# Kernel tuning notes

Hardware: AMD Instinct MI355X
Metric: run time of the kernel (lower is better)

The kernel has to match this reference:

```python
import jax, jax.numpy as jnp
import numpy as np

B, C, H, W = 8, 128, 64, 64
CQK = C // 8


def setup_inputs() -> dict:
    key = jax.random.key(0)
    ks = jax.random.split(key, 7)
    scale = 1.0 / np.sqrt(C)
    return {
        "x": jax.random.normal(ks[0], (B, C, H, W), dtype=jnp.float32),
        "wq": jax.random.normal(ks[1], (CQK, C), dtype=jnp.float32) * scale,
        "bq": jax.random.normal(ks[2], (CQK,), dtype=jnp.float32) * 0.01,
        "wk": jax.random.normal(ks[3], (CQK, C), dtype=jnp.float32) * scale,
        "bk": jax.random.normal(ks[4], (CQK,), dtype=jnp.float32) * 0.01,
        "wv": jax.random.normal(ks[5], (C, C), dtype=jnp.float32) * scale,
        "bv": jax.random.normal(ks[6], (C,), dtype=jnp.float32) * 0.01,
    }


def reference(x, wq, bq, wk, bk, wv, bv):
    b, c, h, w = x.shape
    n = h * w
    xf = x.reshape(b, c, n)                                  # [B,C,N]
    # 1x1 convs == channel matmuls
    q = jnp.einsum('oc,bcn->bon', wq, xf) + bq[:, None]      # [B,C/8,N]
    k = jnp.einsum('oc,bcn->bon', wk, xf) + bk[:, None]      # [B,C/8,N]
    v = jnp.einsum('oc,bcn->bon', wv, xf) + bv[:, None]      # [B,C,N]
    # energy[b,i,j] = <q[:,i], k[:,j]>  (note: NO 1/sqrt(d) scale, per source)
    energy = jnp.einsum('bci,bcj->bij', q, k)                # [B,N,N]
    att = jax.nn.softmax(energy, axis=-1)                    # softmax over j
    # out[b,c,i] = sum_j v[b,c,j] * att[b,i,j]
    out = jnp.einsum('bcj,bij->bci', v, att).reshape(b, c, h, w)
    return out + x
```

## Files before the change

### kernel.cpp

```cpp
#include <hip/hip_runtime.h>
#include <math.h>

#define NB  8
#define NC  128
#define NN  4096
#define NCQ 16
#define BI  64
#define BJ  64
#define WROWS 160

typedef __attribute__((ext_vector_type(8))) short short8v;
typedef __attribute__((ext_vector_type(4))) short short4v;
typedef __attribute__((ext_vector_type(4))) float f32x4;

__device__ __forceinline__ short f2bf(float f) {
    unsigned u = __builtin_bit_cast(unsigned, f);
    u += 0x7fffu + ((u >> 16) & 1u);
    return (short)(u >> 16);
}
__device__ __forceinline__ float bf2f(short h) {
    return __builtin_bit_cast(float, ((unsigned)(unsigned short)h) << 16);
}

__global__ __launch_bounds__(256) void qkv_proj(
    const float* __restrict__ x,
    const float* __restrict__ wq, const float* __restrict__ bq,
    const float* __restrict__ wk, const float* __restrict__ bk,
    const float* __restrict__ wv, const float* __restrict__ bv,
    short* __restrict__ Qo, short* __restrict__ Ko, short* __restrict__ Vo)
{
    __shared__ __align__(16) short wh[WROWS][NC];
    __shared__ __align__(16) short wl[WROWS][NC];
    __shared__ float bias_s[WROWS];

    const int b  = blockIdx.y;
    const int n0 = blockIdx.x * 128;
    const int t  = threadIdx.x;
    const int w  = t >> 6;
    const int l  = t & 63;
    const int lr = l & 15;
    const int g  = l >> 4;

    for (int idx = t; idx < (WROWS * NC) / 4; idx += 256) {
        const int row = idx >> 5;
        const int c4  = (idx & 31) * 4;
        const float* src = (row < 16) ? (wq + row * NC + c4)
                         : (row < 32) ? (wk + (row - 16) * NC + c4)
                                      : (wv + (row - 32) * NC + c4);
        const float4 v = *reinterpret_cast<const float4*>(src);
        short4v h4, l4;
        const float vf[4] = {v.x, v.y, v.z, v.w};
#pragma unroll
        for (int p = 0; p < 4; ++p) {
            const short hi = f2bf(vf[p]);
            h4[p] = hi;
            l4[p] = f2bf(vf[p] - bf2f(hi));
        }
        const int cs = c4 ^ ((row & 7) << 3);
        *reinterpret_cast<short4v*>(&wh[row][cs]) = h4;
        *reinterpret_cast<short4v*>(&wl[row][cs]) = l4;
    }
    for (int i = t; i < WROWS; i += 256)
        bias_s[i] = (i < 16) ? bq[i] : (i < 32) ? bk[i - 16] : bv[i - 32];
    __syncthreads();

    const int col0 = n0 + (2 * w) * 16 + lr;
    const int col1 = col0 + 16;
    const float* xb = x + (size_t)b * NC * NN;

    f32x4 acc[10][2];
#pragma unroll
    for (int rt = 0; rt < 10; ++rt)
#pragma unroll
        for (int c = 0; c < 2; ++c) acc[rt][c] = {0.f, 0.f, 0.f, 0.f};

#pragma unroll
    for (int ks = 0; ks < 4; ++ks) {
        short8v xh0, xl0, xh1, xl1;
        {
            const float* xp0 = xb + (size_t)(32 * ks + 8 * g) * NN + col0;
            const float* xp1 = xb + (size_t)(32 * ks + 8 * g) * NN + col1;
#pragma unroll
            for (int e = 0; e < 8; ++e) {
                const float f0 = xp0[(size_t)e * NN];
                const float f1 = xp1[(size_t)e * NN];
                const short h0 = f2bf(f0), h1 = f2bf(f1);
                xh0[e] = h0; xl0[e] = f2bf(f0 - bf2f(h0));
                xh1[e] = h1; xl1[e] = f2bf(f1 - bf2f(h1));
            }
        }
#pragma unroll
        for (int rt = 0; rt < 10; ++rt) {
            const int row = 16 * rt + lr;
            const int cs  = (32 * ks + 8 * g) ^ ((row & 7) << 3);
            const short8v ah = *reinterpret_cast<const short8v*>(&wh[row][cs]);
            const short8v al = *reinterpret_cast<const short8v*>(&wl[row][cs]);
            acc[rt][0] = __builtin_amdgcn_mfma_f32_16x16x32_bf16(ah, xh0, acc[rt][0], 0, 0, 0);
            acc[rt][0] = __builtin_amdgcn_mfma_f32_16x16x32_bf16(ah, xl0, acc[rt][0], 0, 0, 0);
            acc[rt][0] = __builtin_amdgcn_mfma_f32_16x16x32_bf16(al, xh0, acc[rt][0], 0, 0, 0);
            acc[rt][1] = __builtin_amdgcn_mfma_f32_16x16x32_bf16(ah, xh1, acc[rt][1], 0, 0, 0);
            acc[rt][1] = __builtin_amdgcn_mfma_f32_16x16x32_bf16(ah, xl1, acc[rt][1], 0, 0, 0);
            acc[rt][1] = __builtin_amdgcn_mfma_f32_16x16x32_bf16(al, xh1, acc[rt][1], 0, 0, 0);
        }
    }

#pragma unroll
    for (int rt = 0; rt < 10; ++rt) {
#pragma unroll
        for (int ctx = 0; ctx < 2; ++ctx) {
            const int col = (ctx == 0) ? col0 : col1;
#pragma unroll
            for (int r = 0; r < 4; ++r) {
                const int ch = 16 * rt + 4 * g + r;
                const short o = f2bf(acc[rt][ctx][r] + bias_s[ch]);
                if (rt == 0)
                    Qo[((size_t)b * NCQ + ch) * NN + col] = o;
                else if (rt == 1)
                    Ko[((size_t)b * NCQ + (ch - 16)) * NN + col] = o;
                else
                    Vo[((size_t)b * NC + (ch - 32)) * NN + col] = o;
            }
        }
    }
}

__global__ __launch_bounds__(256) void attn_mfma(
    const short* __restrict__ Q, const short* __restrict__ K,
    const short* __restrict__ V, const float* __restrict__ x,
    float* __restrict__ out)
{
    __shared__ __align__(16) short ksT[2][BJ * 24];
    __shared__ __align__(16) short vsT[2][NC * BJ];
    __shared__ __align__(16) short psT[4][16 * BJ];

    const int b  = blockIdx.y;
    const int i0 = blockIdx.x * BI;
    const int t  = threadIdx.x;
    const int w  = t >> 6;
    const int l  = t & 63;
    const int lr = l & 15;
    const int g  = l >> 4;
    const int swz = (lr & 7) << 3;

    const short* Qb = Q + (size_t)b * NCQ * NN;
    const short* Kb = K + (size_t)b * NCQ * NN;
    const short* Vb = V + (size_t)b * NC * NN;

    const int ig = i0 + 16 * w + lr;

    const short8v kzero = {0, 0, 0, 0, 0, 0, 0, 0};
    const f32x4   fzero = {0.f, 0.f, 0.f, 0.f};

    const int kc  = t >> 4;
    const int kj4 = (t & 15) * 4;
    const int vc0 = t >> 3;
    const int vj8 = (t & 7) * 8;

    short4v kreg;
    short8v vreg0, vreg1, vreg2, vreg3;

#define LOAD_TILE(J0)                                                            \
    {                                                                            \
        kreg  = *reinterpret_cast<const short4v*>(Kb + (size_t)kc * NN + (J0) + kj4); \
        vreg0 = *reinterpret_cast<const short8v*>(Vb + (size_t)(vc0      ) * NN + (J0) + vj8); \
        vreg1 = *reinterpret_cast<const short8v*>(Vb + (size_t)(vc0 + 32 ) * NN + (J0) + vj8); \
        vreg2 = *reinterpret_cast<const short8v*>(Vb + (size_t)(vc0 + 64 ) * NN + (J0) + vj8); \
        vreg3 = *reinterpret_cast<const short8v*>(Vb + (size_t)(vc0 + 96 ) * NN + (J0) + vj8); \
    }
#define WRITE_TILE(BUF)                                                          \
    {                                                                            \
        _Pragma("unroll")                                                        \
        for (int p = 0; p < 4; ++p) ksT[BUF][(kj4 + p) * 24 + kc] = kreg[p];     \
        const int sw0 = vj8 ^ ((vc0 & 7) << 3);                                  \
        *reinterpret_cast<short8v*>(&vsT[BUF][(vc0      ) * BJ + sw0]) = vreg0;  \
        *reinterpret_cast<short8v*>(&vsT[BUF][(vc0 + 32 ) * BJ + sw0]) = vreg1;  \
        *reinterpret_cast<short8v*>(&vsT[BUF][(vc0 + 64 ) * BJ + sw0]) = vreg2;  \
        *reinterpret_cast<short8v*>(&vsT[BUF][(vc0 + 96 ) * BJ + sw0]) = vreg3;  \
    }

    short8v qf = kzero;
    if (g < 2) {
        const short* qp = Qb + (size_t)(8 * g) * NN + ig;
#pragma unroll
        for (int e = 0; e < 8; ++e) qf[e] = qp[(size_t)e * NN];
    }

    float l_run = 0.f;
    f32x4 acc[8];
#pragma unroll
    for (int cb = 0; cb < 8; ++cb) acc[cb] = fzero;

    LOAD_TILE(0)
    WRITE_TILE(0)
    __syncthreads();

    for (int jt = 0; jt < NN / BJ; ++jt) {
        const int cur = jt & 1;
        if (jt < NN / BJ - 1) LOAD_TILE((jt + 1) * BJ)

        f32x4 e0, e1, e2, e3;
#define QK_TILE(ET, TT)                                                          \
        {                                                                        \
            short8v kf = kzero;                                                  \
            if (g < 2)                                                           \
                kf = *reinterpret_cast<const short8v*>(                          \
                        &ksT[cur][(16 * (TT) + lr) * 24 + 8 * g]);               \
            ET = __builtin_amdgcn_mfma_f32_16x16x32_bf16(kf, qf, fzero, 0, 0, 0);\
        }
        QK_TILE(e0, 0) QK_TILE(e1, 1) QK_TILE(e2, 2) QK_TILE(e3, 3)
#undef QK_TILE

        float sum = 0.f;
#pragma unroll
        for (int r = 0; r < 4; ++r) { e0[r] = __expf(e0[r]); sum += e0[r]; }
#pragma unroll
        for (int r = 0; r < 4; ++r) { e1[r] = __expf(e1[r]); sum += e1[r]; }
#pragma unroll
        for (int r = 0; r < 4; ++r) { e2[r] = __expf(e2[r]); sum += e2[r]; }
#pragma unroll
        for (int r = 0; r < 4; ++r) { e3[r] = __expf(e3[r]); sum += e3[r]; }
        sum += __shfl_xor(sum, 16);
        sum += __shfl_xor(sum, 32);
        l_run += sum;

#define P_STORE(ET, TT)                                                           \
        {                                                                         \
            const int jb = 16 * (TT) + 4 * g;                                     \
            unsigned p01 = (unsigned short)f2bf(ET[0]) |                          \
                           ((unsigned)(unsigned short)f2bf(ET[1]) << 16);         \
            unsigned p23 = (unsigned short)f2bf(ET[2]) |                          \
                           ((unsigned)(unsigned short)f2bf(ET[3]) << 16);         \
            *reinterpret_cast<unsigned*>(&psT[w][lr * BJ + ( jb      ^ swz)]) = p01; \
            *reinterpret_cast<unsigned*>(&psT[w][lr * BJ + ((jb + 2) ^ swz)]) = p23; \
        }
        P_STORE(e0, 0) P_STORE(e1, 1) P_STORE(e2, 2) P_STORE(e3, 3)
#undef P_STORE

        __builtin_amdgcn_s_setprio(1);
#pragma unroll
        for (int ks = 0; ks < 2; ++ks) {
            const int jb = (32 * ks + 8 * g) ^ swz;
            const short8v pf = *reinterpret_cast<const short8v*>(&psT[w][lr * BJ + jb]);
#pragma unroll
            for (int cb = 0; cb < 8; ++cb) {
                const short8v vf = *reinterpret_cast<const short8v*>(
                        &vsT[cur][(16 * cb + lr) * BJ + jb]);
                acc[cb] = __builtin_amdgcn_mfma_f32_16x16x32_bf16(vf, pf, acc[cb], 0, 0, 0);
            }
        }
        __builtin_amdgcn_s_setprio(0);

        if (jt < NN / BJ - 1) WRITE_TILE(cur ^ 1)
        __syncthreads();
    }
#undef LOAD_TILE
#undef WRITE_TILE

    const float inv = 1.f / l_run;
#pragma unroll
    for (int cb = 0; cb < 8; ++cb) {
#pragma unroll
        for (int r = 0; r < 4; ++r) {
            const int c = 16 * cb + 4 * g + r;
            const size_t o = ((size_t)b * NC + c) * NN + ig;
            out[o] = acc[cb][r] * inv + x[o];
        }
    }
}

extern "C" void kernel_launch(void* const* d_in, const int* in_sizes, int n_in,
                              void* d_out, int out_size, void* d_ws, size_t ws_size,
                              hipStream_t stream) {
    const float* x  = (const float*)d_in[0];
    const float* wq = (const float*)d_in[1];
    const float* bq = (const float*)d_in[2];
    const float* wk = (const float*)d_in[3];
    const float* bk = (const float*)d_in[4];
    const float* wv = (const float*)d_in[5];
    const float* bv = (const float*)d_in[6];
    float* out = (float*)d_out;

    short* ws = (short*)d_ws;
    short* Qo = ws;
    short* Ko = ws + (size_t)NB * NCQ * NN;
    short* Vo = ws + 2 * (size_t)NB * NCQ * NN;

    dim3 gridp(NN / 128, NB);
    qkv_proj<<<gridp, 256, 0, stream>>>(x, wq, bq, wk, bk, wv, bv, Qo, Ko, Vo);
    dim3 grida(NN / BI, NB);
    attn_mfma<<<grida, 256, 0, stream>>>(Qo, Ko, Vo, x, out);
}
```

Measured before the change: 182.6 us.

## Split weight conversion into its own kernel, stage x in LDS, and skew the PV pipeline

```diff
diff --git a/kernel.cpp b/kernel.cpp
--- a/kernel.cpp
+++ b/kernel.cpp
@@ -7,6 +7,7 @@
 #define NCQ 16
 #define BI  64
 #define BJ  64
+#define NT  (NN / BJ)
 #define WROWS 160
 
 typedef __attribute__((ext_vector_type(8))) short short8v;
@@ -22,104 +23,93 @@
     return __builtin_bit_cast(float, ((unsigned)(unsigned short)h) << 16);
 }
 
-__global__ __launch_bounds__(256) void qkv_proj(
-    const float* __restrict__ x,
+__global__ __launch_bounds__(256) void wconv(
     const float* __restrict__ wq, const float* __restrict__ bq,
     const float* __restrict__ wk, const float* __restrict__ bk,
     const float* __restrict__ wv, const float* __restrict__ bv,
+    short* __restrict__ whg, short* __restrict__ wlg, float* __restrict__ biasg)
+{
+    const int idx = blockIdx.x * 256 + threadIdx.x;
+    if (idx < WROWS * NC) {
+        const int row = idx >> 7, k = idx & 127;
+        const float v = (row < 16) ? wq[row * NC + k]
+                       : (row < 32) ? wk[(row - 16) * NC + k]
+                                    : wv[(row - 32) * NC + k];
+        const short h = f2bf(v);
+        whg[idx] = h;
+        wlg[idx] = f2bf(v - bf2f(h));
+    }
+    if (idx < WROWS)
+        biasg[idx] = (idx < 16) ? bq[idx] : (idx < 32) ? bk[idx - 16] : bv[idx - 32];
+}
+
+__global__ __launch_bounds__(256) void qkv_gemm(
+    const float* __restrict__ x,
+    const short* __restrict__ whg, const short* __restrict__ wlg,
+    const float* __restrict__ biasg,
     short* __restrict__ Qo, short* __restrict__ Ko, short* __restrict__ Vo)
 {
-    __shared__ __align__(16) short wh[WROWS][NC];
-    __shared__ __align__(16) short wl[WROWS][NC];
-    __shared__ float bias_s[WROWS];
+    __shared__ __align__(16) short xsT[2][64][136];
 
     const int b  = blockIdx.y;
-    const int n0 = blockIdx.x * 128;
+    const int n0 = blockIdx.x * 64;
     const int t  = threadIdx.x;
     const int w  = t >> 6;
     const int l  = t & 63;
     const int lr = l & 15;
     const int g  = l >> 4;
 
-    for (int idx = t; idx < (WROWS * NC) / 4; idx += 256) {
-        const int row = idx >> 5;
-        const int c4  = (idx & 31) * 4;
-        const float* src = (row < 16) ? (wq + row * NC + c4)
-                         : (row < 32) ? (wk + (row - 16) * NC + c4)
-                                      : (wv + (row - 32) * NC + c4);
-        const float4 v = *reinterpret_cast<const float4*>(src);
-        short4v h4, l4;
+    const float* xb = x + (size_t)b * NC * NN;
+
+#pragma unroll
+    for (int it = 0; it < 8; ++it) {
+        const int idx4 = t + 256 * it;
+        const int cr = idx4 >> 4;
+        const int j4 = (idx4 & 15) * 4;
+        const float4 v = *reinterpret_cast<const float4*>(xb + (size_t)cr * NN + n0 + j4);
         const float vf[4] = {v.x, v.y, v.z, v.w};
 #pragma unroll
         for (int p = 0; p < 4; ++p) {
-            const short hi = f2bf(vf[p]);
-            h4[p] = hi;
-            l4[p] = f2bf(vf[p] - bf2f(hi));
-        }
-        const int cs = c4 ^ ((row & 7) << 3);
-        *reinterpret_cast<short4v*>(&wh[row][cs]) = h4;
-        *reinterpret_cast<short4v*>(&wl[row][cs]) = l4;
-    }
-    for (int i = t; i < WROWS; i += 256)
-        bias_s[i] = (i < 16) ? bq[i] : (i < 32) ? bk[i - 16] : bv[i - 32];
+            const short h = f2bf(vf[p]);
+            xsT[0][j4 + p][cr] = h;
+            xsT[1][j4 + p][cr] = f2bf(vf[p] - bf2f(h));
+        }
+    }
     __syncthreads();
 
-    const int col0 = n0 + (2 * w) * 16 + lr;
-    const int col1 = col0 + 16;
-    const float* xb = x + (size_t)b * NC * NN;
-
-    f32x4 acc[10][2];
-#pragma unroll
-    for (int rt = 0; rt < 10; ++rt)
-#pragma unroll
-        for (int c = 0; c < 2; ++c) acc[rt][c] = {0.f, 0.f, 0.f, 0.f};
+    const int lc = 16 * w + lr;
+    f32x4 acc[10];
+#pragma unroll
+    for (int rt = 0; rt < 10; ++rt) acc[rt] = {0.f, 0.f, 0.f, 0.f};
 
 #pragma unroll
     for (int ks = 0; ks < 4; ++ks) {
-        short8v xh0, xl0, xh1, xl1;
-        {
-            const float* xp0 = xb + (size_t)(32 * ks + 8 * g) * NN + col0;
-            const float* xp1 = xb + (size_t)(32 * ks + 8 * g) * NN + col1;
-#pragma unroll
-            for (int e = 0; e < 8; ++e) {
-                const float f0 = xp0[(size_t)e * NN];
-                const float f1 = xp1[(size_t)e * NN];
-                const short h0 = f2bf(f0), h1 = f2bf(f1);
-                xh0[e] = h0; xl0[e] = f2bf(f0 - bf2f(h0));
-                xh1[e] = h1; xl1[e] = f2bf(f1 - bf2f(h1));
-            }
-        }
+        const short8v xh = *reinterpret_cast<const short8v*>(&xsT[0][lc][32 * ks + 8 * g]);
+        const short8v xl = *reinterpret_cast<const short8v*>(&xsT[1][lc][32 * ks + 8 * g]);
 #pragma unroll
         for (int rt = 0; rt < 10; ++rt) {
-            const int row = 16 * rt + lr;
-            const int cs  = (32 * ks + 8 * g) ^ ((row & 7) << 3);
-            const short8v ah = *reinterpret_cast<const short8v*>(&wh[row][cs]);
-            const short8v al = *reinterpret_cast<const short8v*>(&wl[row][cs]);
-            acc[rt][0] = __builtin_amdgcn_mfma_f32_16x16x32_bf16(ah, xh0, acc[rt][0], 0, 0, 0);
-            acc[rt][0] = __builtin_amdgcn_mfma_f32_16x16x32_bf16(ah, xl0, acc[rt][0], 0, 0, 0);
-            acc[rt][0] = __builtin_amdgcn_mfma_f32_16x16x32_bf16(al, xh0, acc[rt][0], 0, 0, 0);
-            acc[rt][1] = __builtin_amdgcn_mfma_f32_16x16x32_bf16(ah, xh1, acc[rt][1], 0, 0, 0);
-            acc[rt][1] = __builtin_amdgcn_mfma_f32_16x16x32_bf16(ah, xl1, acc[rt][1], 0, 0, 0);
-            acc[rt][1] = __builtin_amdgcn_mfma_f32_16x16x32_bf16(al, xh1, acc[rt][1], 0, 0, 0);
-        }
-    }
-
+            const int wo = (16 * rt + lr) * NC + 32 * ks + 8 * g;
+            const short8v ah = *reinterpret_cast<const short8v*>(whg + wo);
+            const short8v al = *reinterpret_cast<const short8v*>(wlg + wo);
+            acc[rt] = __builtin_amdgcn_mfma_f32_16x16x32_bf16(ah, xh, acc[rt], 0, 0, 0);
+            acc[rt] = __builtin_amdgcn_mfma_f32_16x16x32_bf16(ah, xl, acc[rt], 0, 0, 0);
+            acc[rt] = __builtin_amdgcn_mfma_f32_16x16x32_bf16(al, xh, acc[rt], 0, 0, 0);
+        }
+    }
+
+    const int col = n0 + lc;
 #pragma unroll
     for (int rt = 0; rt < 10; ++rt) {
 #pragma unroll
-        for (int ctx = 0; ctx < 2; ++ctx) {
-            const int col = (ctx == 0) ? col0 : col1;
-#pragma unroll
-            for (int r = 0; r < 4; ++r) {
-                const int ch = 16 * rt + 4 * g + r;
-                const short o = f2bf(acc[rt][ctx][r] + bias_s[ch]);
-                if (rt == 0)
-                    Qo[((size_t)b * NCQ + ch) * NN + col] = o;
-                else if (rt == 1)
-                    Ko[((size_t)b * NCQ + (ch - 16)) * NN + col] = o;
-                else
-                    Vo[((size_t)b * NC + (ch - 32)) * NN + col] = o;
-            }
+        for (int r = 0; r < 4; ++r) {
+            const int ch = 16 * rt + 4 * g + r;
+            const short o = f2bf(acc[rt][r] + biasg[ch]);
+            if (rt == 0)
+                Qo[((size_t)b * NCQ + ch) * NN + col] = o;
+            else if (rt == 1)
+                Ko[((size_t)b * NCQ + (ch - 16)) * NN + col] = o;
+            else
+                Vo[((size_t)b * NC + (ch - 32)) * NN + col] = o;
         }
     }
 }
@@ -130,8 +120,8 @@
     float* __restrict__ out)
 {
     __shared__ __align__(16) short ksT[2][BJ * 24];
-    __shared__ __align__(16) short vsT[2][NC * BJ];
-    __shared__ __align__(16) short psT[4][16 * BJ];
+    __shared__ __align__(16) short vsT[3][NC * BJ];
+    __shared__ __align__(16) short psT[4][2][16 * BJ];
 
     const int b  = blockIdx.y;
     const int i0 = blockIdx.x * BI;
@@ -167,15 +157,32 @@
         vreg2 = *reinterpret_cast<const short8v*>(Vb + (size_t)(vc0 + 64 ) * NN + (J0) + vj8); \
         vreg3 = *reinterpret_cast<const short8v*>(Vb + (size_t)(vc0 + 96 ) * NN + (J0) + vj8); \
     }
-#define WRITE_TILE(BUF)                                                          \
+#define WRITE_TILE(KB_, VB_)                                                     \
     {                                                                            \
         _Pragma("unroll")                                                        \
-        for (int p = 0; p < 4; ++p) ksT[BUF][(kj4 + p) * 24 + kc] = kreg[p];     \
+        for (int p = 0; p < 4; ++p) ksT[KB_][(kj4 + p) * 24 + kc] = kreg[p];     \
         const int sw0 = vj8 ^ ((vc0 & 7) << 3);                                  \
-        *reinterpret_cast<short8v*>(&vsT[BUF][(vc0      ) * BJ + sw0]) = vreg0;  \
-        *reinterpret_cast<short8v*>(&vsT[BUF][(vc0 + 32 ) * BJ + sw0]) = vreg1;  \
-        *reinterpret_cast<short8v*>(&vsT[BUF][(vc0 + 64 ) * BJ + sw0]) = vreg2;  \
-        *reinterpret_cast<short8v*>(&vsT[BUF][(vc0 + 96 ) * BJ + sw0]) = vreg3;  \
+        *reinterpret_cast<short8v*>(&vsT[VB_][(vc0      ) * BJ + sw0]) = vreg0;  \
+        *reinterpret_cast<short8v*>(&vsT[VB_][(vc0 + 32 ) * BJ + sw0]) = vreg1;  \
+        *reinterpret_cast<short8v*>(&vsT[VB_][(vc0 + 64 ) * BJ + sw0]) = vreg2;  \
+        *reinterpret_cast<short8v*>(&vsT[VB_][(vc0 + 96 ) * BJ + sw0]) = vreg3;  \
+    }
+#define PV_STEP(PB_, VB_)                                                        \
+    {                                                                            \
+        __builtin_amdgcn_s_setprio(1);                                           \
+        _Pragma("unroll")                                                        \
+        for (int ks = 0; ks < 2; ++ks) {                                         \
+            const int jb = (32 * ks + 8 * g) ^ swz;                              \
+            const short8v pf = *reinterpret_cast<const short8v*>(                \
+                    &psT[w][PB_][lr * BJ + jb]);                                 \
+            _Pragma("unroll")                                                    \
+            for (int cb = 0; cb < 8; ++cb) {                                     \
+                const short8v vf = *reinterpret_cast<const short8v*>(            \
+                        &vsT[VB_][(16 * cb + lr) * BJ + jb]);                    \
+                acc[cb] = __builtin_amdgcn_mfma_f32_16x16x32_bf16(vf, pf, acc[cb], 0, 0, 0); \
+            }                                                                    \
+        }                                                                        \
+        __builtin_amdgcn_s_setprio(0);                                           \
     }
 
     short8v qf = kzero;
@@ -191,12 +198,15 @@
     for (int cb = 0; cb < 8; ++cb) acc[cb] = fzero;
 
     LOAD_TILE(0)
-    WRITE_TILE(0)
+    WRITE_TILE(0, 0)
     __syncthreads();
 
-    for (int jt = 0; jt < NN / BJ; ++jt) {
-        const int cur = jt & 1;
-        if (jt < NN / BJ - 1) LOAD_TILE((jt + 1) * BJ)
+    int vwr = 1;
+    int vpv = 0;
+
+    for (int jt = 0; jt < NT; ++jt) {
+        const int kcur = jt & 1;
+        if (jt < NT - 1) LOAD_TILE((jt + 1) * BJ)
 
         f32x4 e0, e1, e2, e3;
 #define QK_TILE(ET, TT)                                                          \
@@ -204,7 +214,7 @@
             short8v kf = kzero;                                                  \
             if (g < 2)                                                           \
                 kf = *reinterpret_cast<const short8v*>(                          \
-                        &ksT[cur][(16 * (TT) + lr) * 24 + 8 * g]);               \
+                        &ksT[kcur][(16 * (TT) + lr) * 24 + 8 * g]);              \
             ET = __builtin_amdgcn_mfma_f32_16x16x32_bf16(kf, qf, fzero, 0, 0, 0);\
         }
         QK_TILE(e0, 0) QK_TILE(e1, 1) QK_TILE(e2, 2) QK_TILE(e3, 3)
@@ -230,31 +240,29 @@
                            ((unsigned)(unsigned short)f2bf(ET[1]) << 16);         \
             unsigned p23 = (unsigned short)f2bf(ET[2]) |                          \
                            ((unsigned)(unsigned short)f2bf(ET[3]) << 16);         \
-            *reinterpret_cast<unsigned*>(&psT[w][lr * BJ + ( jb      ^ swz)]) = p01; \
-            *reinterpret_cast<unsigned*>(&psT[w][lr * BJ + ((jb + 2) ^ swz)]) = p23; \
+            *reinterpret_cast<unsigned*>(&psT[w][kcur][lr * BJ + ( jb      ^ swz)]) = p01; \
+            *reinterpret_cast<unsigned*>(&psT[w][kcur][lr * BJ + ((jb + 2) ^ swz)]) = p23; \
         }
         P_STORE(e0, 0) P_STORE(e1, 1) P_STORE(e2, 2) P_STORE(e3, 3)
 #undef P_STORE
 
-        __builtin_amdgcn_s_setprio(1);
-#pragma unroll
-        for (int ks = 0; ks < 2; ++ks) {
-            const int jb = (32 * ks + 8 * g) ^ swz;
-            const short8v pf = *reinterpret_cast<const short8v*>(&psT[w][lr * BJ + jb]);
-#pragma unroll
-            for (int cb = 0; cb < 8; ++cb) {
-                const short8v vf = *reinterpret_cast<const short8v*>(
-                        &vsT[cur][(16 * cb + lr) * BJ + jb]);
-                acc[cb] = __builtin_amdgcn_mfma_f32_16x16x32_bf16(vf, pf, acc[cb], 0, 0, 0);
-            }
-        }
-        __builtin_amdgcn_s_setprio(0);
-
-        if (jt < NN / BJ - 1) WRITE_TILE(cur ^ 1)
+        if (jt > 0) {
+            PV_STEP(kcur ^ 1, vpv)
+            vpv = (vpv == 2) ? 0 : vpv + 1;
+        }
+
+        if (jt < NT - 1) {
+            WRITE_TILE(kcur ^ 1, vwr)
+            vwr = (vwr == 2) ? 0 : vwr + 1;
+        }
         __syncthreads();
     }
+
+    PV_STEP((NT - 1) & 1, vpv)
+
 #undef LOAD_TILE
 #undef WRITE_TILE
+#undef PV_STEP
 
     const float inv = 1.f / l_run;
 #pragma unroll
@@ -281,12 +289,14 @@
     float* out = (float*)d_out;
 
     short* ws = (short*)d_ws;
-    short* Qo = ws;
-    short* Ko = ws + (size_t)NB * NCQ * NN;
-    short* Vo = ws + 2 * (size_t)NB * NCQ * NN;
-
-    dim3 gridp(NN / 128, NB);
-    qkv_proj<<<gridp, 256, 0, stream>>>(x, wq, bq, wk, bk, wv, bv, Qo, Ko, Vo);
-    dim3 grida(NN / BI, NB);
-    attn_mfma<<<grida, 256, 0, stream>>>(Qo, Ko, Vo, x, out);
-}
+    short* Qo  = ws;
+    short* Ko  = ws + (size_t)NB * NCQ * NN;
+    short* Vo  = ws + 2 * (size_t)NB * NCQ * NN;
+    short* whg = ws + 10 * (size_t)NB * NCQ * NN;
+    short* wlg = whg + WROWS * NC;
+    float* biasg = (float*)(wlg + WROWS * NC);
+
+    wconv<<<dim3(80), 256, 0, stream>>>(wq, bq, wk, bk, wv, bv, whg, wlg, biasg);
+    qkv_gemm<<<dim3(NN / 64, NB), 256, 0, stream>>>(x, whg, wlg, biasg, Qo, Ko, Vo);
+    attn_mfma<<<dim3(NN / BI, NB), 256, 0, stream>>>(Qo, Ko, Vo, x, out);
+}
```

Result: slower. 193.3 us (+5.8%).
